# Optimization experiments

Hardware: AMD Instinct MI355X
Metric: run time of the kernel (lower is better)

The kernel has to match this reference:

```python
import jax, jax.numpy as jnp
import numpy as np

ETA = 1.0
C_STAB = 0.1
SIGMA2 = 512.0  # RBF bandwidth, kernel_args['sigma2']
N_SAMPLE, S, D = 8192, 64, 512


def rbf_kernel(x, sigma2):
    # K[i,j] = exp(-||x_i - x_j||^2 / (2*sigma2)); x: [n, d] -> K: [n, n]
    sq = jnp.sum(x * x, axis=1)
    d2 = sq[:, None] + sq[None, :] - 2.0 * (x @ x.T)
    return jnp.exp(-d2 / (2.0 * sigma2))


def setup_inputs() -> dict:
    key = jax.random.key(0)
    k1, k2, k3 = jax.random.split(key, 3)
    return {
        "input_data": jax.random.normal(k1, (N_SAMPLE, D), dtype=jnp.float32),
        "weight": jax.random.normal(k2, (N_SAMPLE, S), dtype=jnp.float32),
        "inv_lambda_diag": jax.random.normal(k3, (S,), dtype=jnp.float32),
    }


def reference(input_data, weight, inv_lambda_diag):
    K = rbf_kernel(input_data, SIGMA2)          # [n, n]
    E = weight.T @ K                             # [s, n] : e_j for all samples at once
    # loss1 = sum_i e_i^T diag(inv_lambda) e_i, scaled
    loss1 = -jnp.sum(inv_lambda_diag[:, None] * E * E) / (2.0 * ETA ** 2)
    # loss2 = trace(W^T K W) = sum_{s,n} E[s,n] * W[n,s]
    loss2 = jnp.einsum("sn,ns->", E, weight) / (2.0 * ETA)
    L = loss1 + loss2
    return L + (C_STAB / 2.0) * jnp.square(L)
```

## Files before the change

### kernel.cpp

```cpp
#include <hip/hip_runtime.h>
#include <hip/hip_bf16.h>

typedef __bf16 bf16x8 __attribute__((ext_vector_type(8)));
typedef float f32x4 __attribute__((ext_vector_type(4)));
typedef long longx2 __attribute__((ext_vector_type(2)));
typedef int i32x8 __attribute__((ext_vector_type(8)));

#define N 8192
#define D 512
#define NS 64

#define XS_OFF 0
#define WT_OFF (4 * 1024 * 1024)
#define SQ_OFF (WT_OFF + 1024 * 1024)
#define EP_OFF (SQ_OFF + 32 * 1024)
#define SC_OFF (EP_OFF + 8 * 64 * 8192 * 4)

#define BAR() do { asm volatile("s_waitcnt lgkmcnt(0)" ::: "memory"); \
                   __builtin_amdgcn_s_barrier(); } while (0)

__global__ __launch_bounds__(256) void prep(const float* __restrict__ X,
                                            const float* __restrict__ W,
                                            unsigned char* __restrict__ Xs,
                                            float* __restrict__ sq,
                                            __bf16* __restrict__ WTs,
                                            float* __restrict__ Sacc) {
    __shared__ float T[64][65];
    int t = threadIdx.x;
    if (blockIdx.x == 0 && t == 0) {
        Sacc[0] = 0.f; Sacc[1] = 0.f; ((int*)Sacc)[2] = 0;
    }
    if (blockIdx.x < 2048) {
        int row = blockIdx.x * 4 + (t >> 6);
        int l = t & 63;
        const float* src = X + (size_t)row * D + l * 8;
        float4 v0 = *(const float4*)src;
        float4 v1 = *(const float4*)(src + 4);
        int w0 = __builtin_amdgcn_cvt_pk_fp8_f32(v0.x, v0.y, 0, false);
        w0     = __builtin_amdgcn_cvt_pk_fp8_f32(v0.z, v0.w, w0, true);
        int w1 = __builtin_amdgcn_cvt_pk_fp8_f32(v1.x, v1.y, 0, false);
        w1     = __builtin_amdgcn_cvt_pk_fp8_f32(v1.z, v1.w, w1, true);
        uint2 pk = make_uint2((unsigned)w0, (unsigned)w1);
        *(uint2*)(Xs + (size_t)row * 512 + l * 8) = pk;
        float acc = v0.x*v0.x + v0.y*v0.y + v0.z*v0.z + v0.w*v0.w
                  + v1.x*v1.x + v1.y*v1.y + v1.z*v1.z + v1.w*v1.w;
        for (int off = 32; off > 0; off >>= 1) acc += __shfl_down(acc, off);
        if (l == 0) sq[row] = acc;
    } else {
        int i0 = (blockIdx.x - 2048) * 64;
        for (int j = 0; j < 16; ++j) {
            int idx = t + 256 * j;
            T[idx & 63][idx >> 6] = W[(size_t)(i0 + (idx >> 6)) * NS + (idx & 63)];
        }
        __syncthreads();
        for (int h = 0; h < 2; ++h)
            for (int j = 0; j < 8; ++j) {
                int idx = t + 256 * j;
                int s = idx >> 5, il = idx & 31;
                WTs[(size_t)((i0 >> 5) + h) * 2048 + idx] = (__bf16)T[s][h * 32 + il];
            }
    }
}

__global__ __launch_bounds__(256, 2) void kpca_main(
        const unsigned char* __restrict__ Xs, const __bf16* __restrict__ WTs,
        const float* __restrict__ sq, float* __restrict__ Ep) {
    __shared__ __align__(16) unsigned char XiKT[16384];
    __shared__ __align__(16) unsigned char XnHi[4 * 16384];
    unsigned char* Xi = XiKT;

    const int t = threadIdx.x;
    const int w = t >> 6, l = t & 63;
    const int quad = l >> 4, l15 = l & 15;
    const int wm = w >> 1, wn = w & 1;
    const int n0 = blockIdx.x * 128;
    const int ic0 = blockIdx.y * 1024;
    const int sw7 = l15 & 7;

    union U8 { longx2 h[2]; i32x8 v; };

    #pragma unroll 4
    for (int m = 0; m < 16; ++m) {
        int id = m * 256 + t;
        int c = id >> 10, rem = id & 1023;
        int r = rem >> 3, j = rem & 7;
        uint4 v = *(const uint4*)(Xs + (size_t)(n0 + r) * 512 + c * 128 + j * 16);
        *(uint4*)(XnHi + c * 16384 + r * 128 + ((j ^ (r & 7)) << 4)) = v;
    }
    float sqn_v[4];
    #pragma unroll
    for (int nt = 0; nt < 4; ++nt)
        sqn_v[nt] = sq[n0 + wn * 64 + nt * 16 + l15];

    f32x4 accE[4][2];
    #pragma unroll
    for (int st = 0; st < 4; ++st)
        for (int n2 = 0; n2 < 2; ++n2)
            accE[st][n2] = (f32x4){0.f, 0.f, 0.f, 0.f};

    const int rB = t >> 3;
    const int cB = (t & 7) * 16;
    const int swoff = (((t & 7) ^ ((t >> 3) & 7)) << 4);

    const int oswL = (((2 * quad)     ^ sw7) << 4);
    const int oswH = (((2 * quad + 1) ^ sw7) << 4);

    {
        const unsigned char* g = Xs + (size_t)(ic0 + rB) * 512 + cB;
        #pragma unroll
        for (int j = 0; j < 4; ++j)
            *(uint4*)(Xi + (size_t)(j * 32 + rB) * 128 + swoff) =
                *(const uint4*)(g + (size_t)j * 32 * 512);
    }

    uint4 q[4];

    for (int it = 0; it < 8; ++it) {
        const int i0 = ic0 + it * 128;
        f32x4 accG[4][4];
        #pragma unroll
        for (int mt = 0; mt < 4; ++mt)
            for (int nt = 0; nt < 4; ++nt)
                accG[mt][nt] = (f32x4){0.f, 0.f, 0.f, 0.f};

        if (it > 0) {
            BAR();
            #pragma unroll
            for (int j = 0; j < 4; ++j)
                *(uint4*)(Xi + (size_t)(j * 32 + rB) * 128 + swoff) = q[j];
        }

        #pragma unroll
        for (int ks = 0; ks < 4; ++ks) {
            if (ks < 3) {
                const unsigned char* g =
                    Xs + (size_t)(ic0 + it * 128 + rB) * 512 + (ks + 1) * 128 + cB;
                #pragma unroll
                for (int j = 0; j < 4; ++j)
                    q[j] = *(const uint4*)(g + (size_t)j * 32 * 512);
            }
            BAR();

            U8 a[4];
            const unsigned char* abase = Xi + (wm * 64 + l15) * 128;
            #pragma unroll
            for (int mt = 0; mt < 4; ++mt) {
                a[mt].h[0] = *(const longx2*)(abase + mt * 2048 + oswL);
                a[mt].h[1] = *(const longx2*)(abase + mt * 2048 + oswH);
            }
            const unsigned char* bbase = XnHi + ks * 16384 + (wn * 64 + l15) * 128;
            __builtin_amdgcn_s_setprio(1);
            #pragma unroll
            for (int nt = 0; nt < 4; ++nt) {
                U8 bb;
                bb.h[0] = *(const longx2*)(bbase + nt * 2048 + oswL);
                bb.h[1] = *(const longx2*)(bbase + nt * 2048 + oswH);
                #pragma unroll
                for (int mt = 0; mt < 4; ++mt)
                    accG[mt][nt] = __builtin_amdgcn_mfma_scale_f32_16x16x128_f8f6f4(
                        a[mt].v, bb.v, accG[mt][nt],
                        0, 0, 0, 0x7F7F7F7F, 0, 0x7F7F7F7F);
            }
            __builtin_amdgcn_s_setprio(0);

            if (ks < 3) {
                BAR();
                #pragma unroll
                for (int j = 0; j < 4; ++j)
                    *(uint4*)(Xi + (size_t)(j * 32 + rB) * 128 + swoff) = q[j];
            }
        }

        const __bf16* wslab = WTs + (size_t)(i0 >> 5) * 2048;

        auto write_pk = [&]() {
            #pragma unroll
            for (int mt = 0; mt < 4; ++mt) {
                f32x4 si = *(const f32x4*)(sq + i0 + wm * 64 + mt * 16 + quad * 4);
                #pragma unroll
                for (int nt = 0; nt < 4; ++nt) {
                    float sn = sqn_v[nt];
                    union { __bf16 h[4]; uint2 u; } u;
                    #pragma unroll
                    for (int r = 0; r < 4; ++r) {
                        float d2 = si[r] + sn - 2.0f * accG[mt][nt][r];
                        u.h[r] = (__bf16)__expf(d2 * -9.765625e-4f);
                    }
                    int row = wn * 64 + nt * 16 + l15;
                    int blk = mt * 2 + (quad >> 1);
                    *(uint2*)(XiKT + row * 128 + ((blk ^ sw7) << 4) + (quad & 1) * 8)
                        = u.u;
                }
            }
        };

        bf16x8 aw[2][4];
        #pragma unroll
        for (int kc2 = 0; kc2 < 2; ++kc2)
            for (int st = 0; st < 4; ++st)
                aw[kc2][st] = *(const bf16x8*)(wslab + kc2 * 2048 +
                                               (st * 16 + l15) * 32 + quad * 8);

        BAR();
        if (wm == 0) write_pk();
        BAR();
        #pragma unroll
        for (int kc2 = 0; kc2 < 2; ++kc2) {
            bf16x8 bk[2];
            for (int n2 = 0; n2 < 2; ++n2) {
                int row = w * 32 + n2 * 16 + l15;
                bk[n2] = *(const bf16x8*)(XiKT + row * 128 +
                                          (((kc2 * 4 + quad) ^ sw7) << 4));
            }
            #pragma unroll
            for (int st = 0; st < 4; ++st)
                for (int n2 = 0; n2 < 2; ++n2)
                    accE[st][n2] = __builtin_amdgcn_mfma_f32_16x16x32_bf16(
                        aw[kc2][st], bk[n2], accE[st][n2], 0, 0, 0);
        }
        #pragma unroll
        for (int kc2 = 0; kc2 < 2; ++kc2)
            for (int st = 0; st < 4; ++st)
                aw[kc2][st] = *(const bf16x8*)(wslab + (kc2 + 2) * 2048 +
                                               (st * 16 + l15) * 32 + quad * 8);
        BAR();
        if (wm == 1) write_pk();
        if (it < 7) {
            const unsigned char* g =
                Xs + (size_t)(ic0 + (it + 1) * 128 + rB) * 512 + cB;
            #pragma unroll
            for (int j = 0; j < 4; ++j)
                q[j] = *(const uint4*)(g + (size_t)j * 32 * 512);
        }
        BAR();
        #pragma unroll
        for (int kc2 = 0; kc2 < 2; ++kc2) {
            bf16x8 bk[2];
            for (int n2 = 0; n2 < 2; ++n2) {
                int row = w * 32 + n2 * 16 + l15;
                bk[n2] = *(const bf16x8*)(XiKT + row * 128 +
                                          (((kc2 * 4 + quad) ^ sw7) << 4));
            }
            #pragma unroll
            for (int st = 0; st < 4; ++st)
                for (int n2 = 0; n2 < 2; ++n2)
                    accE[st][n2] = __builtin_amdgcn_mfma_f32_16x16x32_bf16(
                        aw[kc2][st], bk[n2], accE[st][n2], 0, 0, 0);
        }
    }

    float* ep = Ep + (size_t)blockIdx.y * (NS * N);
    #pragma unroll
    for (int st = 0; st < 4; ++st)
        for (int n2 = 0; n2 < 2; ++n2)
            for (int r = 0; r < 4; ++r) {
                int s = st * 16 + quad * 4 + r;
                int n = n0 + w * 32 + n2 * 16 + l15;
                ep[(size_t)s * N + n] = accE[st][n2][r];
            }
}

__global__ __launch_bounds__(256) void loss_kernel(const float* __restrict__ Ep,
                                                   const __bf16* __restrict__ WTs,
                                                   const float* __restrict__ lam,
                                                   float* __restrict__ Sacc,
                                                   float* __restrict__ out) {
    int s = blockIdx.x >> 2;
    int nb = (blockIdx.x & 3) * 2048;
    int t = threadIdx.x;
    float a1 = 0.f, a2 = 0.f;
    for (int j = 0; j < 8; ++j) {
        int n = nb + t + j * 256;
        float e = 0.f;
        #pragma unroll
        for (int c = 0; c < 8; ++c)
            e += Ep[(size_t)c * (NS * N) + (size_t)s * N + n];
        a1 += e * e;
        a2 += e * (float)WTs[(size_t)(n >> 5) * 2048 + s * 32 + (n & 31)];
    }
    for (int off = 32; off > 0; off >>= 1) {
        a1 += __shfl_down(a1, off);
        a2 += __shfl_down(a2, off);
    }
    __shared__ float r1[4], r2[4];
    int wv = t >> 6, ln = t & 63;
    if (ln == 0) { r1[wv] = a1; r2[wv] = a2; }
    __syncthreads();
    if (t == 0) {
        atomicAdd(Sacc + 0, lam[s] * (r1[0] + r1[1] + r1[2] + r1[3]));
        atomicAdd(Sacc + 1, r2[0] + r2[1] + r2[2] + r2[3]);
        __threadfence();
        int prev = atomicAdd((int*)Sacc + 2, 1);
        if (prev == 255) {
            __threadfence();
            volatile float* vs = (volatile float*)Sacc;
            float L = 0.5f * (vs[1] - vs[0]);
            out[0] = L + 0.05f * L * L;
        }
    }
}

extern "C" void kernel_launch(void* const* d_in, const int* in_sizes, int n_in,
                              void* d_out, int out_size, void* d_ws, size_t ws_size,
                              hipStream_t stream) {
    const float* X   = (const float*)d_in[0];
    const float* W   = (const float*)d_in[1];
    const float* lam = (const float*)d_in[2];
    float* out = (float*)d_out;
    char* ws = (char*)d_ws;
    unsigned char* Xs = (unsigned char*)(ws + XS_OFF);
    __bf16* WTs = (__bf16*)(ws + WT_OFF);
    float* sq   = (float*)(ws + SQ_OFF);
    float* Ep   = (float*)(ws + EP_OFF);
    float* Sacc = (float*)(ws + SC_OFF);

    prep<<<2048 + 128, 256, 0, stream>>>(X, W, Xs, sq, WTs, Sacc);
    kpca_main<<<dim3(64, 8), 256, 0, stream>>>(Xs, WTs, sq, Ep);
    loss_kernel<<<256, 256, 0, stream>>>(Ep, WTs, lam, Sacc, out);
}
```

Baseline: 165.4 us.

## Double-buffer Xi via direct global-to-LDS loads and keep half of Xn in registers

```diff
diff --git a/kernel.cpp b/kernel.cpp
--- a/kernel.cpp
+++ b/kernel.cpp
@@ -18,6 +18,10 @@
 
 #define BAR() do { asm volatile("s_waitcnt lgkmcnt(0)" ::: "memory"); \
                    __builtin_amdgcn_s_barrier(); } while (0)
+
+#define GLDS(gp, lp) __builtin_amdgcn_global_load_lds(                        \
+    (const __attribute__((address_space(1))) void*)(gp),                      \
+    (__attribute__((address_space(3))) void*)(lp), 16, 0, 0)
 
 __global__ __launch_bounds__(256) void prep(const float* __restrict__ X,
                                             const float* __restrict__ W,
@@ -65,9 +69,9 @@
 __global__ __launch_bounds__(256, 2) void kpca_main(
         const unsigned char* __restrict__ Xs, const __bf16* __restrict__ WTs,
         const float* __restrict__ sq, float* __restrict__ Ep) {
-    __shared__ __align__(16) unsigned char XiKT[16384];
-    __shared__ __align__(16) unsigned char XnHi[4 * 16384];
-    unsigned char* Xi = XiKT;
+    __shared__ __align__(16) unsigned char Xi[2][16384];
+    __shared__ __align__(16) unsigned char XnHi[2][16384];
+    __shared__ __align__(16) unsigned char KTb[16384];
 
     const int t = threadIdx.x;
     const int w = t >> 6, l = t & 63;
@@ -79,13 +83,24 @@
 
     union U8 { longx2 h[2]; i32x8 v; };
 
+    U8 bc[2][4];
+    {
+        const unsigned char* Bb = Xs + (size_t)(n0 + wn * 64 + l15) * 512 + quad * 32;
+        #pragma unroll
+        for (int k2 = 0; k2 < 2; ++k2)
+            #pragma unroll
+            for (int nt = 0; nt < 4; ++nt) {
+                bc[k2][nt].h[0] = *(const longx2*)(Bb + k2 * 128 + nt * 8192);
+                bc[k2][nt].h[1] = *(const longx2*)(Bb + k2 * 128 + nt * 8192 + 16);
+            }
+    }
     #pragma unroll 4
-    for (int m = 0; m < 16; ++m) {
+    for (int m = 0; m < 8; ++m) {
         int id = m * 256 + t;
         int c = id >> 10, rem = id & 1023;
         int r = rem >> 3, j = rem & 7;
-        uint4 v = *(const uint4*)(Xs + (size_t)(n0 + r) * 512 + c * 128 + j * 16);
-        *(uint4*)(XnHi + c * 16384 + r * 128 + ((j ^ (r & 7)) << 4)) = v;
+        uint4 v = *(const uint4*)(Xs + (size_t)(n0 + r) * 512 + 256 + c * 128 + j * 16);
+        *(uint4*)(XnHi[c] + r * 128 + ((j ^ (r & 7)) << 4)) = v;
     }
     float sqn_v[4];
     #pragma unroll
@@ -98,22 +113,16 @@
         for (int n2 = 0; n2 < 2; ++n2)
             accE[st][n2] = (f32x4){0.f, 0.f, 0.f, 0.f};
 
-    const int rB = t >> 3;
-    const int cB = (t & 7) * 16;
-    const int swoff = (((t & 7) ^ ((t >> 3) & 7)) << 4);
+    const int rl = l >> 3;
+    const int sswz = ((l & 7) ^ rl) << 4;
 
     const int oswL = (((2 * quad)     ^ sw7) << 4);
     const int oswH = (((2 * quad + 1) ^ sw7) << 4);
 
-    {
-        const unsigned char* g = Xs + (size_t)(ic0 + rB) * 512 + cB;
-        #pragma unroll
-        for (int j = 0; j < 4; ++j)
-            *(uint4*)(Xi + (size_t)(j * 32 + rB) * 128 + swoff) =
-                *(const uint4*)(g + (size_t)j * 32 * 512);
-    }
-
-    uint4 q[4];
+    #pragma unroll
+    for (int j = 0; j < 4; ++j)
+        GLDS(Xs + (size_t)(ic0 + w * 32 + j * 8 + rl) * 512 + sswz,
+             Xi[0] + w * 4096 + j * 1024);
 
     for (int it = 0; it < 8; ++it) {
         const int i0 = ic0 + it * 128;
@@ -123,57 +132,62 @@
             for (int nt = 0; nt < 4; ++nt)
                 accG[mt][nt] = (f32x4){0.f, 0.f, 0.f, 0.f};
 
-        if (it > 0) {
-            BAR();
-            #pragma unroll
-            for (int j = 0; j < 4; ++j)
-                *(uint4*)(Xi + (size_t)(j * 32 + rB) * 128 + swoff) = q[j];
-        }
-
         #pragma unroll
         for (int ks = 0; ks < 4; ++ks) {
-            if (ks < 3) {
-                const unsigned char* g =
-                    Xs + (size_t)(ic0 + it * 128 + rB) * 512 + (ks + 1) * 128 + cB;
+            __syncthreads();
+            if (ks < 3 || it < 7) {
+                const int ibn = ic0 + ((ks < 3) ? it : it + 1) * 128;
+                const int ksn = (ks + 1) & 3;
                 #pragma unroll
                 for (int j = 0; j < 4; ++j)
-                    q[j] = *(const uint4*)(g + (size_t)j * 32 * 512);
-            }
-            BAR();
-
+                    GLDS(Xs + (size_t)(ibn + w * 32 + j * 8 + rl) * 512 +
+                             ksn * 128 + sswz,
+                         Xi[(ks + 1) & 1] + w * 4096 + j * 1024);
+            }
             U8 a[4];
-            const unsigned char* abase = Xi + (wm * 64 + l15) * 128;
+            const unsigned char* abase = Xi[ks & 1] + (wm * 64 + l15) * 128;
             #pragma unroll
             for (int mt = 0; mt < 4; ++mt) {
                 a[mt].h[0] = *(const longx2*)(abase + mt * 2048 + oswL);
                 a[mt].h[1] = *(const longx2*)(abase + mt * 2048 + oswH);
             }
-            const unsigned char* bbase = XnHi + ks * 16384 + (wn * 64 + l15) * 128;
             __builtin_amdgcn_s_setprio(1);
-            #pragma unroll
-            for (int nt = 0; nt < 4; ++nt) {
-                U8 bb;
-                bb.h[0] = *(const longx2*)(bbase + nt * 2048 + oswL);
-                bb.h[1] = *(const longx2*)(bbase + nt * 2048 + oswH);
-                #pragma unroll
-                for (int mt = 0; mt < 4; ++mt)
-                    accG[mt][nt] = __builtin_amdgcn_mfma_scale_f32_16x16x128_f8f6f4(
-                        a[mt].v, bb.v, accG[mt][nt],
-                        0, 0, 0, 0x7F7F7F7F, 0, 0x7F7F7F7F);
+            if (ks < 2) {
+                #pragma unroll
+                for (int nt = 0; nt < 4; ++nt)
+                    #pragma unroll
+                    for (int mt = 0; mt < 4; ++mt)
+                        accG[mt][nt] = __builtin_amdgcn_mfma_scale_f32_16x16x128_f8f6f4(
+                            a[mt].v, bc[ks][nt].v, accG[mt][nt],
+                            0, 0, 0, 0x7F7F7F7F, 0, 0x7F7F7F7F);
+            } else {
+                const unsigned char* bbase = XnHi[ks - 2] + (wn * 64 + l15) * 128;
+                #pragma unroll
+                for (int nt = 0; nt < 4; ++nt) {
+                    U8 bb;
+                    bb.h[0] = *(const longx2*)(bbase + nt * 2048 + oswL);
+                    bb.h[1] = *(const longx2*)(bbase + nt * 2048 + oswH);
+                    #pragma unroll
+                    for (int mt = 0; mt < 4; ++mt)
+                        accG[mt][nt] = __builtin_amdgcn_mfma_scale_f32_16x16x128_f8f6f4(
+                            a[mt].v, bb.v, accG[mt][nt],
+                            0, 0, 0, 0x7F7F7F7F, 0, 0x7F7F7F7F);
+                }
             }
             __builtin_amdgcn_s_setprio(0);
-
-            if (ks < 3) {
-                BAR();
-                #pragma unroll
-                for (int j = 0; j < 4; ++j)
-                    *(uint4*)(Xi + (size_t)(j * 32 + rB) * 128 + swoff) = q[j];
-            }
         }
 
         const __bf16* wslab = WTs + (size_t)(i0 >> 5) * 2048;
-
-        auto write_pk = [&]() {
+        bf16x8 aw[2][4];
+        #pragma unroll
+        for (int kc2 = 0; kc2 < 2; ++kc2)
+            for (int st = 0; st < 4; ++st)
+                aw[kc2][st] = *(const bf16x8*)(wslab + kc2 * 2048 +
+                                               (st * 16 + l15) * 32 + quad * 8);
+
+        BAR();
+        {
+            unsigned char* dst = (wm == 0) ? KTb : Xi[1];
             #pragma unroll
             for (int mt = 0; mt < 4; ++mt) {
                 f32x4 si = *(const f32x4*)(sq + i0 + wm * 64 + mt * 16 + quad * 4);
@@ -188,64 +202,34 @@
                     }
                     int row = wn * 64 + nt * 16 + l15;
                     int blk = mt * 2 + (quad >> 1);
-                    *(uint2*)(XiKT + row * 128 + ((blk ^ sw7) << 4) + (quad & 1) * 8)
+                    *(uint2*)(dst + row * 128 + ((blk ^ sw7) << 4) + (quad & 1) * 8)
                         = u.u;
                 }
             }
-        };
-
-        bf16x8 aw[2][4];
-        #pragma unroll
-        for (int kc2 = 0; kc2 < 2; ++kc2)
-            for (int st = 0; st < 4; ++st)
-                aw[kc2][st] = *(const bf16x8*)(wslab + kc2 * 2048 +
-                                               (st * 16 + l15) * 32 + quad * 8);
-
+        }
         BAR();
-        if (wm == 0) write_pk();
-        BAR();
-        #pragma unroll
-        for (int kc2 = 0; kc2 < 2; ++kc2) {
+        #pragma unroll
+        for (int kc = 0; kc < 4; ++kc) {
+            if (kc == 2) {
+                #pragma unroll
+                for (int kc2 = 0; kc2 < 2; ++kc2)
+                    for (int st = 0; st < 4; ++st)
+                        aw[kc2][st] = *(const bf16x8*)(wslab + (kc2 + 2) * 2048 +
+                                                       (st * 16 + l15) * 32 + quad * 8);
+            }
+            const unsigned char* srcb = (kc < 2) ? KTb : Xi[1];
             bf16x8 bk[2];
+            #pragma unroll
             for (int n2 = 0; n2 < 2; ++n2) {
                 int row = w * 32 + n2 * 16 + l15;
-                bk[n2] = *(const bf16x8*)(XiKT + row * 128 +
-                                          (((kc2 * 4 + quad) ^ sw7) << 4));
+                bk[n2] = *(const bf16x8*)(srcb + row * 128 +
+                                          ((((kc & 1) * 4 + quad) ^ sw7) << 4));
             }
             #pragma unroll
             for (int st = 0; st < 4; ++st)
                 for (int n2 = 0; n2 < 2; ++n2)
                     accE[st][n2] = __builtin_amdgcn_mfma_f32_16x16x32_bf16(
-                        aw[kc2][st], bk[n2], accE[st][n2], 0, 0, 0);
-        }
-        #pragma unroll
-        for (int kc2 = 0; kc2 < 2; ++kc2)
-            for (int st = 0; st < 4; ++st)
-                aw[kc2][st] = *(const bf16x8*)(wslab + (kc2 + 2) * 2048 +
-                                               (st * 16 + l15) * 32 + quad * 8);
-        BAR();
-        if (wm == 1) write_pk();
-        if (it < 7) {
-            const unsigned char* g =
-                Xs + (size_t)(ic0 + (it + 1) * 128 + rB) * 512 + cB;
-            #pragma unroll
-            for (int j = 0; j < 4; ++j)
-                q[j] = *(const uint4*)(g + (size_t)j * 32 * 512);
-        }
-        BAR();
-        #pragma unroll
-        for (int kc2 = 0; kc2 < 2; ++kc2) {
-            bf16x8 bk[2];
-            for (int n2 = 0; n2 < 2; ++n2) {
-                int row = w * 32 + n2 * 16 + l15;
-                bk[n2] = *(const bf16x8*)(XiKT + row * 128 +
-                                          (((kc2 * 4 + quad) ^ sw7) << 4));
-            }
-            #pragma unroll
-            for (int st = 0; st < 4; ++st)
-                for (int n2 = 0; n2 < 2; ++n2)
-                    accE[st][n2] = __builtin_amdgcn_mfma_f32_16x16x32_bf16(
-                        aw[kc2][st], bk[n2], accE[st][n2], 0, 0, 0);
+                        aw[kc & 1][st], bk[n2], accE[st][n2], 0, 0, 0);
         }
     }
 
```

Measured after the change: 175.3 us. +6.0%, slower.
